# Kernel tuning notes

Hardware: AMD Instinct MI355X
Metric: run time of the kernel (lower is better)

The kernel has to match this reference:

```python
import jax, jax.numpy as jnp
import numpy as np

B, T = 2048, 512
H1, H2, H3 = 100, 60, 30


def _glorot(key, shape, fan):
    bound = 1.0 / np.sqrt(fan)
    return jax.random.uniform(key, shape, jnp.float32, -bound, bound)


def setup_inputs() -> dict:
    key = jax.random.key(0)
    ks = jax.random.split(key, 17)
    inp = {"x": jax.random.normal(ks[0], (B, T, 2), jnp.float32)}
    # layer 1: input 2 -> hidden 100
    inp["W_ih1"] = _glorot(ks[1], (H1, 2), H1)
    inp["W_hh1"] = _glorot(ks[2], (H1, H1), H1)
    inp["b_ih1"] = _glorot(ks[3], (H1,), H1)
    inp["b_hh1"] = _glorot(ks[4], (H1,), H1)
    # layer 2: 100 -> 60
    inp["W_ih2"] = _glorot(ks[5], (H2, H1), H2)
    inp["W_hh2"] = _glorot(ks[6], (H2, H2), H2)
    inp["b_ih2"] = _glorot(ks[7], (H2,), H2)
    inp["b_hh2"] = _glorot(ks[8], (H2,), H2)
    # layer 3: 60 -> 30
    inp["W_ih3"] = _glorot(ks[9], (H3, H2), H3)
    inp["W_hh3"] = _glorot(ks[10], (H3, H3), H3)
    inp["b_ih3"] = _glorot(ks[11], (H3,), H3)
    inp["b_hh3"] = _glorot(ks[12], (H3,), H3)
    # heads
    inp["W_o1"] = _glorot(ks[13], (10, H3), 10)
    inp["b_o1"] = _glorot(ks[14], (10,), 10)
    inp["W_o2"] = _glorot(ks[15], (2, 10), 2)
    inp["b_o2"] = _glorot(ks[16], (2,), 2)
    return inp


def rnn_layer(x, W_ih, W_hh, b_ih, b_hh):
    # x: [B, T, in]; precompute the time-parallel input projection once
    xp = jnp.einsum("bti,hi->bth", x, W_ih) + (b_ih + b_hh)  # [B, T, H]
    h0 = jnp.zeros((x.shape[0], W_hh.shape[0]), x.dtype)

    def step(h, xt):  # xt: [B, H]
        h = jnp.tanh(xt + h @ W_hh.T)
        return h, h

    _, ys = jax.lax.scan(step, h0, jnp.swapaxes(xp, 0, 1))  # [T, B, H]
    return jnp.swapaxes(ys, 0, 1)  # [B, T, H]


def reference(x, W_ih1, W_hh1, b_ih1, b_hh1, W_ih2, W_hh2, b_ih2, b_hh2,
              W_ih3, W_hh3, b_ih3, b_hh3, W_o1, b_o1, W_o2, b_o2):
    h = rnn_layer(x, W_ih1, W_hh1, b_ih1, b_hh1)
    h = rnn_layer(h, W_ih2, W_hh2, b_ih2, b_hh2)
    h = rnn_layer(h, W_ih3, W_hh3, b_ih3, b_hh3)
    o = jnp.einsum("bth,oh->bto", h, W_o1) + b_o1
    return jnp.einsum("bto,po->btp", o, W_o2) + b_o2  # [B, T, 2]
```

## Files before the change

### kernel.cpp

```cpp
#include <hip/hip_runtime.h>

typedef _Float16 v8hf __attribute__((ext_vector_type(8)));
typedef float    v4f  __attribute__((ext_vector_type(4)));

#define MFMA16(a, b, c) __builtin_amdgcn_mfma_f32_16x16x32_f16((a), (b), (c), 0, 0, 0)

#define TT 512
#define BT 16
#define NTH 448

__shared__ __align__(16) _Float16 h1b[2][BT][136];
__shared__ __align__(16) _Float16 h2b[2][BT][72];
__shared__ __align__(16) _Float16 h3b[2][BT][40];
__shared__ __align__(16) _Float16 xst[TT][2 * BT];

__device__ __forceinline__ float fast_tanh(float z) {
    z = fminf(15.f, fmaxf(-15.f, z));
    float e = __expf(2.f * z);
    return 1.f - 2.f * __builtin_amdgcn_rcpf(e + 1.f);
}

__global__ __launch_bounds__(NTH)
void rnn3_pipe(const float* __restrict__ xg,
               const float* __restrict__ Wih1, const float* __restrict__ Whh1,
               const float* __restrict__ bih1, const float* __restrict__ bhh1,
               const float* __restrict__ Wih2, const float* __restrict__ Whh2,
               const float* __restrict__ bih2, const float* __restrict__ bhh2,
               const float* __restrict__ Wih3, const float* __restrict__ Whh3,
               const float* __restrict__ bih3, const float* __restrict__ bhh3,
               const float* __restrict__ Wo1,  const float* __restrict__ bo1,
               const float* __restrict__ Wo2,  const float* __restrict__ bo2,
               float* __restrict__ outg)
{
    const int tid   = threadIdx.x;
    const int lane  = tid & 63;
    const int wid   = tid >> 6;
    const int col   = lane & 15;
    const int g     = lane >> 4;
    const int bbase = blockIdx.x * BT;

    {
        _Float16* z1 = &h1b[0][0][0];
        for (int i = tid; i < 2 * BT * 136; i += NTH) z1[i] = (_Float16)0.f;
        _Float16* z2 = &h2b[0][0][0];
        for (int i = tid; i < 2 * BT * 72; i += NTH) z2[i] = (_Float16)0.f;
        _Float16* z3 = &h3b[0][0][0];
        for (int i = tid; i < 2 * BT * 40; i += NTH) z3[i] = (_Float16)0.f;
        for (int i = tid; i < BT * TT * 2; i += NTH) {
            float v = xg[(size_t)bbase * (TT * 2) + i];
            int b = i >> 10, r = i & 1023, t = r >> 1, c = r & 1;
            xst[t][b * 2 + c] = (_Float16)v;
        }
    }

    v8hf f0[4] = {}, f1[4] = {}, f2[2] = {}, f3[2] = {};
    v8hf wbo = {};
    float bA = 0.f, bB = 0.f, beff = 0.f;

    auto ldW = [&](const float* W, int rows, int cols, int j, int kt) -> v8hf {
        v8hf r;
        #pragma unroll
        for (int e = 0; e < 8; ++e) {
            const int k = kt * 32 + g * 8 + e;
            float v = (j < rows && k < cols) ? W[j * cols + k] : 0.f;
            r[e] = (_Float16)v;
        }
        return r;
    };
    auto ldW1 = [&](int j, int kt) -> v8hf {
        v8hf r;
        #pragma unroll
        for (int e = 0; e < 8; ++e) {
            const int k = kt * 32 + g * 8 + e;
            float v = 0.f;
            if (j < 100) {
                if (k < 100)            v = Whh1[j * 100 + k];
                else if (k == 112)      v = Wih1[j * 2];
                else if (k == 113)      v = Wih1[j * 2 + 1];
            }
            r[e] = (_Float16)v;
        }
        return r;
    };

    if (wid < 3) {
        const int ja = 16 * (2 * wid) + col, jb = ja + 16;
        #pragma unroll
        for (int kt = 0; kt < 4; ++kt) { f0[kt] = ldW1(ja, kt); f1[kt] = ldW1(jb, kt); }
        bA = (ja < 100) ? bih1[ja] + bhh1[ja] : 0.f;
        bB = (jb < 100) ? bih1[jb] + bhh1[jb] : 0.f;
    } else if (wid == 3) {
        const int j = 96 + col;
        #pragma unroll
        for (int kt = 0; kt < 4; ++kt) f0[kt] = ldW1(j, kt);
        bA = (j < 100) ? bih1[j] + bhh1[j] : 0.f;
        #pragma unroll
        for (int e = 0; e < 8; ++e) {
            const int k = g * 8 + e;
            float v = 0.f;
            if (col < 2 && k < 30) {
                #pragma unroll
                for (int u = 0; u < 10; ++u) v += Wo2[col * 10 + u] * Wo1[u * 30 + k];
            }
            wbo[e] = (_Float16)v;
        }
        if (col < 2) {
            float bv = bo2[col];
            #pragma unroll
            for (int u = 0; u < 10; ++u) bv += Wo2[col * 10 + u] * bo1[u];
            beff = bv;
        }
    } else if (wid < 6) {
        const int ja = 16 * (2 * (wid - 4)) + col, jb = ja + 16;
        #pragma unroll
        for (int kt = 0; kt < 4; ++kt) { f0[kt] = ldW(Wih2, 60, 100, ja, kt); f1[kt] = ldW(Wih2, 60, 100, jb, kt); }
        #pragma unroll
        for (int kt = 0; kt < 2; ++kt) { f2[kt] = ldW(Whh2, 60, 60, ja, kt); f3[kt] = ldW(Whh2, 60, 60, jb, kt); }
        bA = (ja < 60) ? bih2[ja] + bhh2[ja] : 0.f;
        bB = (jb < 60) ? bih2[jb] + bhh2[jb] : 0.f;
    } else {
        const int ja = col, jb = col + 16;
        #pragma unroll
        for (int kt = 0; kt < 2; ++kt) { f0[kt] = ldW(Wih3, 30, 60, ja, kt); f1[kt] = ldW(Wih3, 30, 60, jb, kt); }
        f2[0] = ldW(Whh3, 30, 30, ja, 0);
        f3[0] = ldW(Whh3, 30, 30, jb, 0);
        bA = (ja < 30) ? bih3[ja] + bhh3[ja] : 0.f;
        bB = (jb < 30) ? bih3[jb] + bhh3[jb] : 0.f;
    }

    __syncthreads();
    if (tid < BT)
        *(unsigned*)&h1b[0][tid][112] = *(const unsigned*)&xst[0][tid * 2];
    __syncthreads();

    for (int s = 0; s < TT + 3; ++s) {
        const int rp = s & 1, wp = rp ^ 1;

        if (wid < 3) {
            if (s < TT) {
                const _Float16* hp = &h1b[rp][col][0];
                v8hf a0 = *(const v8hf*)(hp +      g * 8);
                v8hf a1 = *(const v8hf*)(hp + 32 + g * 8);
                v8hf a2 = *(const v8hf*)(hp + 64 + g * 8);
                v8hf a3 = *(const v8hf*)(hp + 96 + g * 8);
                v4f p0 = {bA, bA, bA, bA}, q0 = {0.f, 0.f, 0.f, 0.f};
                v4f p1 = {bB, bB, bB, bB}, q1 = {0.f, 0.f, 0.f, 0.f};
                p0 = MFMA16(a0, f0[0], p0); q0 = MFMA16(a1, f0[1], q0);
                p0 = MFMA16(a2, f0[2], p0); q0 = MFMA16(a3, f0[3], q0);
                p1 = MFMA16(a0, f1[0], p1); q1 = MFMA16(a1, f1[1], q1);
                p1 = MFMA16(a2, f1[2], p1); q1 = MFMA16(a3, f1[3], q1);
                const int j0 = 32 * wid + col;
                #pragma unroll
                for (int i = 0; i < 4; ++i) {
                    h1b[wp][4 * g + i][j0]      = (_Float16)fast_tanh(p0[i] + q0[i]);
                    h1b[wp][4 * g + i][j0 + 16] = (_Float16)fast_tanh(p1[i] + q1[i]);
                }
            }
        } else if (wid == 3) {
            if (s < TT - 1 && lane < BT)
                *(unsigned*)&h1b[wp][lane][112] = *(const unsigned*)&xst[s + 1][2 * lane];
            if (s < TT) {
                const _Float16* hp = &h1b[rp][col][0];
                v8hf a0 = *(const v8hf*)(hp +      g * 8);
                v8hf a1 = *(const v8hf*)(hp + 32 + g * 8);
                v8hf a2 = *(const v8hf*)(hp + 64 + g * 8);
                v8hf a3 = *(const v8hf*)(hp + 96 + g * 8);
                v4f p0 = {bA, bA, bA, bA}, q0 = {0.f, 0.f, 0.f, 0.f};
                p0 = MFMA16(a0, f0[0], p0); q0 = MFMA16(a1, f0[1], q0);
                p0 = MFMA16(a2, f0[2], p0); q0 = MFMA16(a3, f0[3], q0);
                #pragma unroll
                for (int i = 0; i < 4; ++i)
                    h1b[wp][4 * g + i][96 + col] = (_Float16)fast_tanh(p0[i] + q0[i]);
            }
            if (s >= 3) {
                const _Float16* hp = &h3b[rp][col][0];
                v8hf a = *(const v8hf*)(hp + g * 8);
                v4f o = {beff, beff, beff, beff};
                o = MFMA16(a, wbo, o);
                if (col < 2) {
                    #pragma unroll
                    for (int i = 0; i < 4; ++i)
                        outg[(((size_t)(bbase + 4 * g + i)) * TT + (s - 3)) * 2 + col] = o[i];
                }
            }
        } else if (wid < 6) {
            if (s >= 1 && s <= TT) {
                const _Float16* hp1 = &h1b[rp][col][0];
                const _Float16* hp2 = &h2b[wp][col][0];
                v8hf a0 = *(const v8hf*)(hp1 +      g * 8);
                v8hf a1 = *(const v8hf*)(hp1 + 32 + g * 8);
                v8hf a2 = *(const v8hf*)(hp1 + 64 + g * 8);
                v8hf a3 = *(const v8hf*)(hp1 + 96 + g * 8);
                v8hf c0 = *(const v8hf*)(hp2 +      g * 8);
                v8hf c1 = *(const v8hf*)(hp2 + 32 + g * 8);
                v4f p0 = {bA, bA, bA, bA}, q0 = {0.f, 0.f, 0.f, 0.f};
                v4f p1 = {bB, bB, bB, bB}, q1 = {0.f, 0.f, 0.f, 0.f};
                p0 = MFMA16(a0, f0[0], p0); q0 = MFMA16(a1, f0[1], q0);
                p0 = MFMA16(a2, f0[2], p0); q0 = MFMA16(a3, f0[3], q0);
                p0 = MFMA16(c0, f2[0], p0); q0 = MFMA16(c1, f2[1], q0);
                p1 = MFMA16(a0, f1[0], p1); q1 = MFMA16(a1, f1[1], q1);
                p1 = MFMA16(a2, f1[2], p1); q1 = MFMA16(a3, f1[3], q1);
                p1 = MFMA16(c0, f3[0], p1); q1 = MFMA16(c1, f3[1], q1);
                const int j0 = 32 * (wid - 4) + col;
                #pragma unroll
                for (int i = 0; i < 4; ++i) {
                    h2b[rp][4 * g + i][j0]      = (_Float16)fast_tanh(p0[i] + q0[i]);
                    h2b[rp][4 * g + i][j0 + 16] = (_Float16)fast_tanh(p1[i] + q1[i]);
                }
            }
        } else {
            if (s >= 2 && s <= TT + 1) {
                const _Float16* hp2 = &h2b[wp][col][0];
                const _Float16* hp3 = &h3b[rp][col][0];
                v8hf a0 = *(const v8hf*)(hp2 +      g * 8);
                v8hf a1 = *(const v8hf*)(hp2 + 32 + g * 8);
                v8hf c0 = *(const v8hf*)(hp3 +      g * 8);
                v4f p0 = {bA, bA, bA, bA}, q0 = {0.f, 0.f, 0.f, 0.f};
                v4f p1 = {bB, bB, bB, bB}, q1 = {0.f, 0.f, 0.f, 0.f};
                p0 = MFMA16(a0, f0[0], p0); q0 = MFMA16(a1, f0[1], q0);
                p0 = MFMA16(c0, f2[0], p0);
                p1 = MFMA16(a0, f1[0], p1); q1 = MFMA16(a1, f1[1], q1);
                p1 = MFMA16(c0, f3[0], p1);
                #pragma unroll
                for (int i = 0; i < 4; ++i) {
                    h3b[wp][4 * g + i][col]      = (_Float16)fast_tanh(p0[i] + q0[i]);
                    h3b[wp][4 * g + i][col + 16] = (_Float16)fast_tanh(p1[i] + q1[i]);
                }
            }
        }
        __syncthreads();
    }
}

extern "C" void kernel_launch(void* const* d_in, const int* in_sizes, int n_in,
                              void* d_out, int out_size, void* d_ws, size_t ws_size,
                              hipStream_t stream) {
    (void)in_sizes; (void)n_in; (void)d_ws; (void)ws_size; (void)out_size;
    const float* x     = (const float*)d_in[0];
    const float* W_ih1 = (const float*)d_in[1];
    const float* W_hh1 = (const float*)d_in[2];
    const float* b_ih1 = (const float*)d_in[3];
    const float* b_hh1 = (const float*)d_in[4];
    const float* W_ih2 = (const float*)d_in[5];
    const float* W_hh2 = (const float*)d_in[6];
    const float* b_ih2 = (const float*)d_in[7];
    const float* b_hh2 = (const float*)d_in[8];
    const float* W_ih3 = (const float*)d_in[9];
    const float* W_hh3 = (const float*)d_in[10];
    const float* b_ih3 = (const float*)d_in[11];
    const float* b_hh3 = (const float*)d_in[12];
    const float* W_o1  = (const float*)d_in[13];
    const float* b_o1  = (const float*)d_in[14];
    const float* W_o2  = (const float*)d_in[15];
    const float* b_o2  = (const float*)d_in[16];
    float* out = (float*)d_out;

    rnn3_pipe<<<2048 / BT, NTH, 0, stream>>>(
        x, W_ih1, W_hh1, b_ih1, b_hh1,
        W_ih2, W_hh2, b_ih2, b_hh2,
        W_ih3, W_hh3, b_ih3, b_hh3,
        W_o1, b_o1, W_o2, b_o2, out);
}
```

Baseline: 314.6 us.

## Repack three-layer RNN pipeline onto four balanced waves with batched tanh and output ring

Moves the work from seven wavefronts onto four, so each wave now runs several MFMA tiles across layers 1–3. This shrinks the per-step barrier group and spreads the MFMA load more evenly. The tanh is rewritten to handle four values with a single reciprocal via exp2. Outputs are buffered in a shared-memory ring and written to global memory as coalesced float4 stores every 64 steps. In exchange each wave does more serial work per step and holds more registers, and the shared reciprocal can lose accuracy when the factors grow large.

```diff
diff --git a/kernel.cpp b/kernel.cpp
--- a/kernel.cpp
+++ b/kernel.cpp
@@ -7,30 +7,47 @@
 
 #define TT 512
 #define BT 16
-#define NTH 448
+#define NTH 256
 
 __shared__ __align__(16) _Float16 h1b[2][BT][136];
 __shared__ __align__(16) _Float16 h2b[2][BT][72];
 __shared__ __align__(16) _Float16 h3b[2][BT][40];
 __shared__ __align__(16) _Float16 xst[TT][2 * BT];
-
-__device__ __forceinline__ float fast_tanh(float z) {
-    z = fminf(15.f, fmaxf(-15.f, z));
-    float e = __expf(2.f * z);
-    return 1.f - 2.f * __builtin_amdgcn_rcpf(e + 1.f);
+__shared__ __align__(16) float    oring[BT][64][2];
+
+__device__ __forceinline__ v4f tanh4(v4f r) {
+    const float KS = 2.8853900817779268f;
+    const float CL = 13.8498724f;
+    float z0 = fminf(CL, fmaxf(-CL, r[0] * KS));
+    float z1 = fminf(CL, fmaxf(-CL, r[1] * KS));
+    float z2 = fminf(CL, fmaxf(-CL, r[2] * KS));
+    float z3 = fminf(CL, fmaxf(-CL, r[3] * KS));
+    float a0 = __builtin_amdgcn_exp2f(z0) + 1.f;
+    float a1 = __builtin_amdgcn_exp2f(z1) + 1.f;
+    float a2 = __builtin_amdgcn_exp2f(z2) + 1.f;
+    float a3 = __builtin_amdgcn_exp2f(z3) + 1.f;
+    float P = a0 * a1, Q = a2 * a3;
+    float R = __builtin_amdgcn_rcpf(P * Q);
+    float iP = Q * R, iQ = P * R;
+    v4f t;
+    t[0] = 1.f - 2.f * (a1 * iP);
+    t[1] = 1.f - 2.f * (a0 * iP);
+    t[2] = 1.f - 2.f * (a3 * iQ);
+    t[3] = 1.f - 2.f * (a2 * iQ);
+    return t;
 }
 
 __global__ __launch_bounds__(NTH)
-void rnn3_pipe(const float* __restrict__ xg,
-               const float* __restrict__ Wih1, const float* __restrict__ Whh1,
-               const float* __restrict__ bih1, const float* __restrict__ bhh1,
-               const float* __restrict__ Wih2, const float* __restrict__ Whh2,
-               const float* __restrict__ bih2, const float* __restrict__ bhh2,
-               const float* __restrict__ Wih3, const float* __restrict__ Whh3,
-               const float* __restrict__ bih3, const float* __restrict__ bhh3,
-               const float* __restrict__ Wo1,  const float* __restrict__ bo1,
-               const float* __restrict__ Wo2,  const float* __restrict__ bo2,
-               float* __restrict__ outg)
+void rnn3_w4(const float* __restrict__ xg,
+             const float* __restrict__ Wih1, const float* __restrict__ Whh1,
+             const float* __restrict__ bih1, const float* __restrict__ bhh1,
+             const float* __restrict__ Wih2, const float* __restrict__ Whh2,
+             const float* __restrict__ bih2, const float* __restrict__ bhh2,
+             const float* __restrict__ Wih3, const float* __restrict__ Whh3,
+             const float* __restrict__ bih3, const float* __restrict__ bhh3,
+             const float* __restrict__ Wo1,  const float* __restrict__ bo1,
+             const float* __restrict__ Wo2,  const float* __restrict__ bo2,
+             float* __restrict__ outg)
 {
     const int tid   = threadIdx.x;
     const int lane  = tid & 63;
@@ -53,9 +70,10 @@
         }
     }
 
-    v8hf f0[4] = {}, f1[4] = {}, f2[2] = {}, f3[2] = {};
-    v8hf wbo = {};
-    float bA = 0.f, bB = 0.f, beff = 0.f;
+    v8hf F[16];
+    #pragma unroll
+    for (int i = 0; i < 16; ++i) F[i] = (v8hf)(_Float16)0.f;
+    float bb0 = 0.f, bb1 = 0.f, bb2 = 0.f, bb3 = 0.f;
 
     auto ldW = [&](const float* W, int rows, int cols, int j, int kt) -> v8hf {
         v8hf r;
@@ -74,26 +92,36 @@
             const int k = kt * 32 + g * 8 + e;
             float v = 0.f;
             if (j < 100) {
-                if (k < 100)            v = Whh1[j * 100 + k];
-                else if (k == 112)      v = Wih1[j * 2];
-                else if (k == 113)      v = Wih1[j * 2 + 1];
+                if (k < 100)       v = Whh1[j * 100 + k];
+                else if (k == 112) v = Wih1[j * 2];
+                else if (k == 113) v = Wih1[j * 2 + 1];
             }
             r[e] = (_Float16)v;
         }
         return r;
     };
-
-    if (wid < 3) {
-        const int ja = 16 * (2 * wid) + col, jb = ja + 16;
-        #pragma unroll
-        for (int kt = 0; kt < 4; ++kt) { f0[kt] = ldW1(ja, kt); f1[kt] = ldW1(jb, kt); }
-        bA = (ja < 100) ? bih1[ja] + bhh1[ja] : 0.f;
-        bB = (jb < 100) ? bih1[jb] + bhh1[jb] : 0.f;
-    } else if (wid == 3) {
-        const int j = 96 + col;
-        #pragma unroll
-        for (int kt = 0; kt < 4; ++kt) f0[kt] = ldW1(j, kt);
-        bA = (j < 100) ? bih1[j] + bhh1[j] : 0.f;
+    auto bL1 = [&](int j) -> float { return (j < 100) ? bih1[j] + bhh1[j] : 0.f; };
+    auto bL2 = [&](int j) -> float { return (j < 60) ? bih2[j] + bhh2[j] : 0.f; };
+    auto bL3 = [&](int j) -> float { return (j < 30) ? bih3[j] + bhh3[j] : 0.f; };
+
+    if (wid == 0) {
+        #pragma unroll
+        for (int kt = 0; kt < 4; ++kt) {
+            F[0 + kt] = ldW1(col, kt);
+            F[4 + kt] = ldW1(col + 16, kt);
+            F[8 + kt] = ldW1(col + 32, kt);
+        }
+        F[12] = ldW(Wih3, 30, 60, col + 16, 0);
+        F[13] = ldW(Wih3, 30, 60, col + 16, 1);
+        F[14] = ldW(Whh3, 30, 30, col + 16, 0);
+        bb0 = bL1(col); bb1 = bL1(col + 16); bb2 = bL1(col + 32); bb3 = bL3(col + 16);
+    } else if (wid == 1) {
+        #pragma unroll
+        for (int kt = 0; kt < 4; ++kt) {
+            F[0 + kt] = ldW1(col + 48, kt);
+            F[4 + kt] = ldW1(col + 64, kt);
+            F[8 + kt] = ldW1(col + 80, kt);
+        }
         #pragma unroll
         for (int e = 0; e < 8; ++e) {
             const int k = g * 8 + e;
@@ -102,30 +130,37 @@
                 #pragma unroll
                 for (int u = 0; u < 10; ++u) v += Wo2[col * 10 + u] * Wo1[u * 30 + k];
             }
-            wbo[e] = (_Float16)v;
-        }
+            F[12][e] = (_Float16)v;
+        }
+        bb0 = bL1(col + 48); bb1 = bL1(col + 64); bb2 = bL1(col + 80);
         if (col < 2) {
             float bv = bo2[col];
             #pragma unroll
             for (int u = 0; u < 10; ++u) bv += Wo2[col * 10 + u] * bo1[u];
-            beff = bv;
-        }
-    } else if (wid < 6) {
-        const int ja = 16 * (2 * (wid - 4)) + col, jb = ja + 16;
-        #pragma unroll
-        for (int kt = 0; kt < 4; ++kt) { f0[kt] = ldW(Wih2, 60, 100, ja, kt); f1[kt] = ldW(Wih2, 60, 100, jb, kt); }
-        #pragma unroll
-        for (int kt = 0; kt < 2; ++kt) { f2[kt] = ldW(Whh2, 60, 60, ja, kt); f3[kt] = ldW(Whh2, 60, 60, jb, kt); }
-        bA = (ja < 60) ? bih2[ja] + bhh2[ja] : 0.f;
-        bB = (jb < 60) ? bih2[jb] + bhh2[jb] : 0.f;
+            bb3 = bv;
+        }
+    } else if (wid == 2) {
+        #pragma unroll
+        for (int kt = 0; kt < 4; ++kt) {
+            F[0 + kt] = ldW(Wih2, 60, 100, col, kt);
+            F[6 + kt] = ldW(Wih2, 60, 100, col + 16, kt);
+        }
+        F[4]  = ldW(Whh2, 60, 60, col, 0);       F[5]  = ldW(Whh2, 60, 60, col, 1);
+        F[10] = ldW(Whh2, 60, 60, col + 16, 0);  F[11] = ldW(Whh2, 60, 60, col + 16, 1);
+        F[12] = ldW(Wih3, 30, 60, col, 0);
+        F[13] = ldW(Wih3, 30, 60, col, 1);
+        F[14] = ldW(Whh3, 30, 30, col, 0);
+        bb0 = bL2(col); bb1 = bL2(col + 16); bb2 = bL3(col);
     } else {
-        const int ja = col, jb = col + 16;
-        #pragma unroll
-        for (int kt = 0; kt < 2; ++kt) { f0[kt] = ldW(Wih3, 30, 60, ja, kt); f1[kt] = ldW(Wih3, 30, 60, jb, kt); }
-        f2[0] = ldW(Whh3, 30, 30, ja, 0);
-        f3[0] = ldW(Whh3, 30, 30, jb, 0);
-        bA = (ja < 30) ? bih3[ja] + bhh3[ja] : 0.f;
-        bB = (jb < 30) ? bih3[jb] + bhh3[jb] : 0.f;
+        #pragma unroll
+        for (int kt = 0; kt < 4; ++kt) {
+            F[0 + kt]  = ldW1(col + 96, kt);
+            F[4 + kt]  = ldW(Wih2, 60, 100, col + 32, kt);
+            F[10 + kt] = ldW(Wih2, 60, 100, col + 48, kt);
+        }
+        F[8]  = ldW(Whh2, 60, 60, col + 32, 0);  F[9]  = ldW(Whh2, 60, 60, col + 32, 1);
+        F[14] = ldW(Whh2, 60, 60, col + 48, 0);  F[15] = ldW(Whh2, 60, 60, col + 48, 1);
+        bb0 = bL1(col + 96); bb1 = bL2(col + 32); bb2 = bL2(col + 48);
     }
 
     __syncthreads();
@@ -133,99 +168,96 @@
         *(unsigned*)&h1b[0][tid][112] = *(const unsigned*)&xst[0][tid * 2];
     __syncthreads();
 
+#define WR_H1(r, jw) { _Pragma("unroll") for (int i = 0; i < 4; ++i) h1b[wp][4*g+i][jw] = (_Float16)(r)[i]; }
+#define WR_H2(r, jw) { _Pragma("unroll") for (int i = 0; i < 4; ++i) h2b[rp][4*g+i][jw] = (_Float16)(r)[i]; }
+#define WR_H3(r, jw) { _Pragma("unroll") for (int i = 0; i < 4; ++i) h3b[wp][4*g+i][jw] = (_Float16)(r)[i]; }
+
+#define L1_TILE(f0, f1, f2, f3, bias, jw) { \
+    v4f p = {bias, bias, bias, bias}, q = {0.f, 0.f, 0.f, 0.f}; \
+    p = MFMA16(A0, f0, p); q = MFMA16(A1, f1, q); \
+    p = MFMA16(A2, f2, p); q = MFMA16(A3, f3, q); \
+    v4f r = tanh4(p + q); WR_H1(r, jw); }
+
+#define L2_TILE(f0, f1, f2, f3, f4, f5, bias, jw) { \
+    v4f p = {bias, bias, bias, bias}, q = {0.f, 0.f, 0.f, 0.f}; \
+    p = MFMA16(A0, f0, p); q = MFMA16(A1, f1, q); \
+    p = MFMA16(A2, f2, p); q = MFMA16(A3, f3, q); \
+    p = MFMA16(B0, f4, p); q = MFMA16(B1, f5, q); \
+    v4f r = tanh4(p + q); WR_H2(r, jw); }
+
+#define L3_TILE(f0, f1, f2, bias, jw) { \
+    v4f p = {bias, bias, bias, bias}, q = {0.f, 0.f, 0.f, 0.f}; \
+    p = MFMA16(B0, f0, p); q = MFMA16(B1, f1, q); \
+    p = MFMA16(C0, f2, p); \
+    v4f r = tanh4(p + q); WR_H3(r, jw); }
+
     for (int s = 0; s < TT + 3; ++s) {
         const int rp = s & 1, wp = rp ^ 1;
-
-        if (wid < 3) {
+        const _Float16* h1p = &h1b[rp][col][g * 8];
+        const _Float16* h2p = &h2b[wp][col][g * 8];
+        const _Float16* h3p = &h3b[rp][col][g * 8];
+
+        if (wid == 0) {
+            v8hf A0 = *(const v8hf*)(h1p);      v8hf A1 = *(const v8hf*)(h1p + 32);
+            v8hf A2 = *(const v8hf*)(h1p + 64); v8hf A3 = *(const v8hf*)(h1p + 96);
+            v8hf B0 = *(const v8hf*)(h2p);      v8hf B1 = *(const v8hf*)(h2p + 32);
+            v8hf C0 = *(const v8hf*)(h3p);
             if (s < TT) {
-                const _Float16* hp = &h1b[rp][col][0];
-                v8hf a0 = *(const v8hf*)(hp +      g * 8);
-                v8hf a1 = *(const v8hf*)(hp + 32 + g * 8);
-                v8hf a2 = *(const v8hf*)(hp + 64 + g * 8);
-                v8hf a3 = *(const v8hf*)(hp + 96 + g * 8);
-                v4f p0 = {bA, bA, bA, bA}, q0 = {0.f, 0.f, 0.f, 0.f};
-                v4f p1 = {bB, bB, bB, bB}, q1 = {0.f, 0.f, 0.f, 0.f};
-                p0 = MFMA16(a0, f0[0], p0); q0 = MFMA16(a1, f0[1], q0);
-                p0 = MFMA16(a2, f0[2], p0); q0 = MFMA16(a3, f0[3], q0);
-                p1 = MFMA16(a0, f1[0], p1); q1 = MFMA16(a1, f1[1], q1);
-                p1 = MFMA16(a2, f1[2], p1); q1 = MFMA16(a3, f1[3], q1);
-                const int j0 = 32 * wid + col;
-                #pragma unroll
-                for (int i = 0; i < 4; ++i) {
-                    h1b[wp][4 * g + i][j0]      = (_Float16)fast_tanh(p0[i] + q0[i]);
-                    h1b[wp][4 * g + i][j0 + 16] = (_Float16)fast_tanh(p1[i] + q1[i]);
-                }
-            }
-        } else if (wid == 3) {
-            if (s < TT - 1 && lane < BT)
-                *(unsigned*)&h1b[wp][lane][112] = *(const unsigned*)&xst[s + 1][2 * lane];
+                L1_TILE(F[0], F[1], F[2], F[3],   bb0, col);
+                L1_TILE(F[4], F[5], F[6], F[7],   bb1, col + 16);
+                L1_TILE(F[8], F[9], F[10], F[11], bb2, col + 32);
+            }
+            if (s >= 2 && s <= TT + 1) L3_TILE(F[12], F[13], F[14], bb3, col + 16);
+        } else if (wid == 1) {
+            v8hf A0 = *(const v8hf*)(h1p);      v8hf A1 = *(const v8hf*)(h1p + 32);
+            v8hf A2 = *(const v8hf*)(h1p + 64); v8hf A3 = *(const v8hf*)(h1p + 96);
+            v8hf C0 = *(const v8hf*)(h3p);
             if (s < TT) {
-                const _Float16* hp = &h1b[rp][col][0];
-                v8hf a0 = *(const v8hf*)(hp +      g * 8);
-                v8hf a1 = *(const v8hf*)(hp + 32 + g * 8);
-                v8hf a2 = *(const v8hf*)(hp + 64 + g * 8);
-                v8hf a3 = *(const v8hf*)(hp + 96 + g * 8);
-                v4f p0 = {bA, bA, bA, bA}, q0 = {0.f, 0.f, 0.f, 0.f};
-                p0 = MFMA16(a0, f0[0], p0); q0 = MFMA16(a1, f0[1], q0);
-                p0 = MFMA16(a2, f0[2], p0); q0 = MFMA16(a3, f0[3], q0);
-                #pragma unroll
-                for (int i = 0; i < 4; ++i)
-                    h1b[wp][4 * g + i][96 + col] = (_Float16)fast_tanh(p0[i] + q0[i]);
+                L1_TILE(F[0], F[1], F[2], F[3],   bb0, col + 48);
+                L1_TILE(F[4], F[5], F[6], F[7],   bb1, col + 64);
+                L1_TILE(F[8], F[9], F[10], F[11], bb2, col + 80);
             }
             if (s >= 3) {
-                const _Float16* hp = &h3b[rp][col][0];
-                v8hf a = *(const v8hf*)(hp + g * 8);
-                v4f o = {beff, beff, beff, beff};
-                o = MFMA16(a, wbo, o);
+                const int t = s - 3;
+                v4f o = {bb3, bb3, bb3, bb3};
+                o = MFMA16(C0, F[12], o);
                 if (col < 2) {
                     #pragma unroll
-                    for (int i = 0; i < 4; ++i)
-                        outg[(((size_t)(bbase + 4 * g + i)) * TT + (s - 3)) * 2 + col] = o[i];
+                    for (int i = 0; i < 4; ++i) oring[4 * g + i][t & 63][col] = o[i];
                 }
-            }
-        } else if (wid < 6) {
+                if ((t & 63) == 63) {
+                    const int tbase = t - 63;
+                    const float4* ring4 = (const float4*)&oring[0][0][0];
+                    #pragma unroll
+                    for (int jj = 0; jj < 8; ++jj) {
+                        const int f = lane + 64 * jj;
+                        const int b = f >> 5, k = f & 31;
+                        float4 v = ring4[f];
+                        *(float4*)(outg + ((size_t)(bbase + b) * TT + tbase) * 2 + 4 * k) = v;
+                    }
+                }
+            }
+        } else if (wid == 2) {
+            v8hf A0 = *(const v8hf*)(h1p);      v8hf A1 = *(const v8hf*)(h1p + 32);
+            v8hf A2 = *(const v8hf*)(h1p + 64); v8hf A3 = *(const v8hf*)(h1p + 96);
+            v8hf B0 = *(const v8hf*)(h2p);      v8hf B1 = *(const v8hf*)(h2p + 32);
+            v8hf C0 = *(const v8hf*)(h3p);
             if (s >= 1 && s <= TT) {
-                const _Float16* hp1 = &h1b[rp][col][0];
-                const _Float16* hp2 = &h2b[wp][col][0];
-                v8hf a0 = *(const v8hf*)(hp1 +      g * 8);
-                v8hf a1 = *(const v8hf*)(hp1 + 32 + g * 8);
-                v8hf a2 = *(const v8hf*)(hp1 + 64 + g * 8);
-                v8hf a3 = *(const v8hf*)(hp1 + 96 + g * 8);
-                v8hf c0 = *(const v8hf*)(hp2 +      g * 8);
-                v8hf c1 = *(const v8hf*)(hp2 + 32 + g * 8);
-                v4f p0 = {bA, bA, bA, bA}, q0 = {0.f, 0.f, 0.f, 0.f};
-                v4f p1 = {bB, bB, bB, bB}, q1 = {0.f, 0.f, 0.f, 0.f};
-                p0 = MFMA16(a0, f0[0], p0); q0 = MFMA16(a1, f0[1], q0);
-                p0 = MFMA16(a2, f0[2], p0); q0 = MFMA16(a3, f0[3], q0);
-                p0 = MFMA16(c0, f2[0], p0); q0 = MFMA16(c1, f2[1], q0);
-                p1 = MFMA16(a0, f1[0], p1); q1 = MFMA16(a1, f1[1], q1);
-                p1 = MFMA16(a2, f1[2], p1); q1 = MFMA16(a3, f1[3], q1);
-                p1 = MFMA16(c0, f3[0], p1); q1 = MFMA16(c1, f3[1], q1);
-                const int j0 = 32 * (wid - 4) + col;
-                #pragma unroll
-                for (int i = 0; i < 4; ++i) {
-                    h2b[rp][4 * g + i][j0]      = (_Float16)fast_tanh(p0[i] + q0[i]);
-                    h2b[rp][4 * g + i][j0 + 16] = (_Float16)fast_tanh(p1[i] + q1[i]);
-                }
-            }
+                L2_TILE(F[0], F[1], F[2], F[3], F[4], F[5],   bb0, col);
+                L2_TILE(F[6], F[7], F[8], F[9], F[10], F[11], bb1, col + 16);
+            }
+            if (s >= 2 && s <= TT + 1) L3_TILE(F[12], F[13], F[14], bb2, col);
         } else {
-            if (s >= 2 && s <= TT + 1) {
-                const _Float16* hp2 = &h2b[wp][col][0];
-                const _Float16* hp3 = &h3b[rp][col][0];
-                v8hf a0 = *(const v8hf*)(hp2 +      g * 8);
-                v8hf a1 = *(const v8hf*)(hp2 + 32 + g * 8);
-                v8hf c0 = *(const v8hf*)(hp3 +      g * 8);
-                v4f p0 = {bA, bA, bA, bA}, q0 = {0.f, 0.f, 0.f, 0.f};
-                v4f p1 = {bB, bB, bB, bB}, q1 = {0.f, 0.f, 0.f, 0.f};
-                p0 = MFMA16(a0, f0[0], p0); q0 = MFMA16(a1, f0[1], q0);
-                p0 = MFMA16(c0, f2[0], p0);
-                p1 = MFMA16(a0, f1[0], p1); q1 = MFMA16(a1, f1[1], q1);
-                p1 = MFMA16(c0, f3[0], p1);
-                #pragma unroll
-                for (int i = 0; i < 4; ++i) {
-                    h3b[wp][4 * g + i][col]      = (_Float16)fast_tanh(p0[i] + q0[i]);
-                    h3b[wp][4 * g + i][col + 16] = (_Float16)fast_tanh(p1[i] + q1[i]);
-                }
+            if (lane < BT && s < TT - 1)
+                *(unsigned*)&h1b[wp][lane][112] = *(const unsigned*)&xst[s + 1][2 * lane];
+            v8hf A0 = *(const v8hf*)(h1p);      v8hf A1 = *(const v8hf*)(h1p + 32);
+            v8hf A2 = *(const v8hf*)(h1p + 64); v8hf A3 = *(const v8hf*)(h1p + 96);
+            v8hf B0 = *(const v8hf*)(h2p);      v8hf B1 = *(const v8hf*)(h2p + 32);
+            if (s < TT)
+                L1_TILE(F[0], F[1], F[2], F[3], bb0, col + 96);
+            if (s >= 1 && s <= TT) {
+                L2_TILE(F[4], F[5], F[6], F[7], F[8], F[9],     bb1, col + 32);
+                L2_TILE(F[10], F[11], F[12], F[13], F[14], F[15], bb2, col + 48);
             }
         }
         __syncthreads();
@@ -255,7 +287,7 @@
     const float* b_o2  = (const float*)d_in[16];
     float* out = (float*)d_out;
 
-    rnn3_pipe<<<2048 / BT, NTH, 0, stream>>>(
+    rnn3_w4<<<2048 / BT, NTH, 0, stream>>>(
         x, W_ih1, W_hh1, b_ih1, b_hh1,
         W_ih2, W_hh2, b_ih2, b_hh2,
         W_ih3, W_hh3, b_ih3, b_hh3,
```

Measured after the change: 376.2 us. 19.6% more time.
